# Performance work log

Measured on AMD Instinct MI355X. Metric: run time of the kernel, lower is better.

## Reference

```python
import jax, jax.numpy as jnp
import numpy as np
from jax import lax

B, CIN, HID, T, H, W = 4, 16, 16, 31, 128, 128


def setup_inputs() -> dict:
    key = jax.random.key(0)
    k1, k2 = jax.random.split(key)
    X = jax.random.normal(k1, (B, CIN, T, H, W), dtype=jnp.float32)
    # conv weight: Conv3d(in=16, out=4*hidden=64, k=3, pad=1), fan-in scaled
    fan_in = CIN * 27
    Wt = jax.random.normal(k2, (4 * HID, CIN, 3, 3, 3), dtype=jnp.float32) / np.sqrt(fan_in)
    b = jnp.zeros((4 * HID,), dtype=jnp.float32)
    return {"X": X, "W": Wt, "b": b}


def reference(X, W, b):
    # conv step: [B, 4*HID, T, H, W]
    gates = lax.conv_general_dilated(
        X, W, window_strides=(1, 1, 1), padding="SAME",
        dimension_numbers=("NCDHW", "OIDHW", "NCDHW"))
    gates = gates + b[None, :, None, None, None]
    Z, F, O, I = jnp.split(gates, 4, axis=1)
    Z = jnp.tanh(Z)
    F = jax.nn.sigmoid(F)
    O = jax.nn.sigmoid(O)
    I = jax.nn.sigmoid(I)

    # linear recurrence over time (axis=2), forward direction:
    # c_t = f_t * c_{t-1} + i_t * z_t  (c_{-1} = 0), h_t = o_t * c_t
    Zt = jnp.moveaxis(Z, 2, 0)  # [T, B, HID, H, W]
    Ft = jnp.moveaxis(F, 2, 0)
    Ot = jnp.moveaxis(O, 2, 0)
    It = jnp.moveaxis(I, 2, 0)

    def step(c, zfio):
        z, f, o, i = zfio
        c_ = f * c + i * z
        return c_, o * c_

    c0 = jnp.zeros_like(Zt[0])
    _, hs = lax.scan(step, c0, (Zt, Ft, Ot, It))
    return jnp.moveaxis(hs, 0, 2)  # [B, HID, T, H, W]
```

## Files before the change

### kernel.cpp

```cpp
#include <hip/hip_runtime.h>
#include <math.h>

#define Bn   4
#define CINn 16
#define HIDn 16
#define Tn   31
#define Hn   128
#define Wn   128

#define NS   14

typedef _Float16 half8 __attribute__((ext_vector_type(8)));
typedef float    f32x4 __attribute__((ext_vector_type(4)));

constexpr int KDt[28] = {0,0,0,0,0,0,0,0,0, 1,1,1,1,1,1,1,1,1, 2,2,2,2,2,2,2,2,2, 2};
constexpr int KHt[28] = {0,0,0,1,1,1,2,2,2, 0,0,0,1,1,1,2,2,2, 0,0,0,1,1,1,2,2,2, 2};
constexpr int KWt[28] = {0,1,2,0,1,2,0,1,2, 0,1,2,0,1,2,0,1,2, 0,1,2,0,1,2,0,1,2, 2};

__device__ __forceinline__ float sigmoidf_(float x) { return 1.f / (1.f + __expf(-x)); }
__device__ __forceinline__ float tanhf_(float x)    { return 2.f / (1.f + __expf(-2.f * x)) - 1.f; }

__global__ void repack_wa_kernel(const float* __restrict__ W, _Float16* __restrict__ WA) {
    int idx = blockIdx.x * blockDim.x + threadIdx.x;
    if (idx >= NS * 4 * 64 * 8) return;
    int j    = idx & 7;
    int lane = (idx >> 3) & 63;
    int m    = (idx >> 9) & 3;
    int s    = idx >> 11;
    int g    = lane >> 4;
    int tap  = 2 * s + (g >> 1);
    int cin  = (g & 1) * 8 + j;
    int oc   = m * 16 + (lane & 15);
    float v  = (tap < 27) ? W[(size_t)(oc * CINn + cin) * 27 + tap] : 0.f;
    WA[idx] = (_Float16)v;
}

#define POSB    32
#define ROWF    (130*POSB)
#define SLOTF   (3*ROWF)
#define LDSF    (4*SLOTF)
#define XH_OFF  65536
#define SLICE_B (Hn*Wn*CINn*2)
#define WS_NEED ((size_t)XH_OFF + (size_t)Bn*Tn*SLICE_B)

__global__ __launch_bounds__(256)
void transpose_x_kernel(const float* __restrict__ X, _Float16* __restrict__ Xh) {
    int i   = blockIdx.x * 256 + threadIdx.x;
    int pos = i & 16383;
    int bu  = i >> 14;
    int b   = bu / 31;
    int u   = bu - b * 31;
    const float* src = X + ((size_t)(b * CINn) * Tn + u) * 16384 + pos;
    half8 h0, h1;
    #pragma unroll
    for (int c = 0; c < 8; c++) h0[c] = (_Float16)src[(size_t)c * (Tn * 16384)];
    #pragma unroll
    for (int c = 0; c < 8; c++) h1[c] = (_Float16)src[(size_t)(c + 8) * (Tn * 16384)];
    half8* dst = (half8*)(Xh + (size_t)i * 16);
    dst[0] = h0; dst[1] = h1;
}

__global__ __launch_bounds__(256, 2)
void qrnn_xh_kernel(const _Float16* __restrict__ Xh, const _Float16* __restrict__ WA,
                    const float* __restrict__ bias, float* __restrict__ out) {
    __shared__ __align__(16) char smem[LDSF];

    const int tid  = threadIdx.x;
    const int lane = tid & 63;
    const int wv   = tid >> 6;

    const int swz = (blockIdx.x & 7) * 64 + (blockIdx.x >> 3);
    const int b = swz >> 7;
    const int h = swz & 127;

    const size_t strideT = (size_t)Hn * Wn;
    const size_t strideC = (size_t)Tn * strideT;

    const int lane15  = lane & 15;
    const int g       = lane >> 4;
    const int ghi     = g >> 1;
    const int e       = g & 1;
    const int laneoff = lane15 * POSB + e * 16;
    const int wbase   = wv * 32;

    float bz[4], bfv[4], bov[4], biv[4];
    #pragma unroll
    for (int r = 0; r < 4; r++) {
        int hid = g * 4 + r;
        bz[r]  = bias[hid];
        bfv[r] = bias[HIDn + hid];
        bov[r] = bias[2 * HIDn + hid];
        biv[r] = bias[3 * HIDn + hid];
    }

    const char* XhB = (const char*)Xh + (size_t)b * Tn * SLICE_B;
    bool own[2], inb[2]; int soff[2], loff[2];
    #pragma unroll
    for (int k = 0; k < 2; k++) {
        int p  = tid + (k << 8);
        own[k] = (p < 3 * 130);
        int r    = (p >= 260) ? 2 : (p >= 130) ? 1 : 0;
        int wpos = p - r * 130;
        int hr = h - 1 + r;
        int wa = wpos - 1;
        inb[k]  = own[k] && (hr >= 0) && (hr < Hn) && (wa >= 0) && (wa < Wn);
        soff[k] = (hr * Wn + wa) * 32;
        loff[k] = r * ROWF + wpos * POSB;
    }

    half8 pfA[2], pfB[2];

    auto issue = [&](int u) {
        const bool uok = (u >= 0) && (u < Tn);
        #pragma unroll
        for (int k = 0; k < 2; k++) {
            half8 a = {}, c = {};
            if (uok && inb[k]) {
                const char* s = XhB + (size_t)u * SLICE_B + soff[k];
                a = *reinterpret_cast<const half8*>(s);
                c = *reinterpret_cast<const half8*>(s + 16);
            }
            pfA[k] = a; pfB[k] = c;
        }
    };
    auto commit = [&](int u) {
        char* sl = smem + (u & 3) * SLOTF;
        #pragma unroll
        for (int k = 0; k < 2; k++) if (own[k]) {
            *reinterpret_cast<half8*>(sl + loff[k])      = pfA[k];
            *reinterpret_cast<half8*>(sl + loff[k] + 16) = pfB[k];
        }
    };

    {
        half8 z = {};
        #pragma unroll
        for (int k = 0; k < 2; k++) if (own[k]) {
            *reinterpret_cast<half8*>(smem + 3 * SLOTF + loff[k])      = z;
            *reinterpret_cast<half8*>(smem + 3 * SLOTF + loff[k] + 16) = z;
        }
    }
    issue(0);
    commit(0);
    issue(1);

    float cst[2][4];
    #pragma unroll
    for (int n = 0; n < 2; n++)
        #pragma unroll
        for (int r = 0; r < 4; r++) cst[n][r] = 0.f;

    float* outb = out + (size_t)b * HIDn * strideC + (size_t)h * Wn + wbase + lane15;

    for (int t = 0; t < Tn; t++) {
        commit(t + 1);
        __syncthreads();
        issue(t + 2);

        const int sb[3] = { ((t + 3) & 3) * SLOTF, (t & 3) * SLOTF, ((t + 1) & 3) * SLOTF };

        f32x4 acc[2][4];
        #pragma unroll
        for (int n = 0; n < 2; n++)
            #pragma unroll
            for (int m = 0; m < 4; m++) acc[n][m] = (f32x4)(0.f);

        #pragma unroll
        for (int s = 0; s < NS; s++) {
            const half8 a0 = *reinterpret_cast<const half8*>(WA + ((size_t)(s * 4 + 0) * 64 + lane) * 8);
            const half8 a1 = *reinterpret_cast<const half8*>(WA + ((size_t)(s * 4 + 1) * 64 + lane) * 8);
            const half8 a2 = *reinterpret_cast<const half8*>(WA + ((size_t)(s * 4 + 2) * 64 + lane) * 8);
            const half8 a3 = *reinterpret_cast<const half8*>(WA + ((size_t)(s * 4 + 3) * 64 + lane) * 8);

            const int tA = 2 * s, tB = 2 * s + 1;
            const int offA = sb[KDt[tA]] + KHt[tA] * ROWF + KWt[tA] * POSB;
            const int offB = sb[KDt[tB]] + KHt[tB] * ROWF + KWt[tB] * POSB;
            const int off  = (ghi ? offB : offA) + laneoff;

            #pragma unroll
            for (int n = 0; n < 2; n++) {
                const half8 bf = *reinterpret_cast<const half8*>(
                    smem + off + (wbase + n * 16) * POSB);
                acc[n][0] = __builtin_amdgcn_mfma_f32_16x16x32_f16(a0, bf, acc[n][0], 0, 0, 0);
                acc[n][1] = __builtin_amdgcn_mfma_f32_16x16x32_f16(a1, bf, acc[n][1], 0, 0, 0);
                acc[n][2] = __builtin_amdgcn_mfma_f32_16x16x32_f16(a2, bf, acc[n][2], 0, 0, 0);
                acc[n][3] = __builtin_amdgcn_mfma_f32_16x16x32_f16(a3, bf, acc[n][3], 0, 0, 0);
            }
        }

        #pragma unroll
        for (int n = 0; n < 2; n++) {
            #pragma unroll
            for (int r = 0; r < 4; r++) {
                float z = tanhf_   (acc[n][0][r] + bz[r]);
                float f = sigmoidf_(acc[n][1][r] + bfv[r]);
                float o = sigmoidf_(acc[n][2][r] + bov[r]);
                float i = sigmoidf_(acc[n][3][r] + biv[r]);
                float c = f * cst[n][r] + i * z;
                cst[n][r] = c;
                outb[(size_t)(g * 4 + r) * strideC + (size_t)t * strideT + n * 16] = o * c;
            }
        }
    }
}

#define WSTR  48
#define ROWB  (130*WSTR)
#define SLOT3 (3*ROWB)
#define LDS3  (3*SLOT3)

__global__ __launch_bounds__(256, 2)
void qrnn_fb_kernel(const float* __restrict__ X, const _Float16* __restrict__ WA,
                    const float* __restrict__ bias, float* __restrict__ out) {
    __shared__ __align__(16) char smem[LDS3];
    const int tid  = threadIdx.x;
    const int lane = tid & 63;
    const int wv   = tid >> 6;
    const int swz = (blockIdx.x & 7) * 64 + (blockIdx.x >> 3);
    const int b = swz >> 7;
    const int h = swz & 127;
    const size_t strideT = (size_t)Hn * Wn;
    const size_t strideC = (size_t)Tn * strideT;
    const float* Xb = X + (size_t)b * CINn * strideC;
    const int lane15  = lane & 15;
    const int g       = lane >> 4;
    const int ghi     = g >> 1;
    const int laneoff = lane15 * WSTR + (g & 1) * 16;
    const int wbase   = wv * 32;
    float bz[4], bfv[4], bov[4], biv[4];
    #pragma unroll
    for (int r = 0; r < 4; r++) {
        int hid = g * 4 + r;
        bz[r] = bias[hid]; bfv[r] = bias[HIDn + hid];
        bov[r] = bias[2 * HIDn + hid]; biv[r] = bias[3 * HIDn + hid];
    }
    auto stage = [&](int u, int s) {
        const bool uok = (u >= 0) && (u < Tn);
        for (int p = tid; p < 3 * 130; p += 256) {
            int row  = (p >= 260) ? 2 : (p >= 130) ? 1 : 0;
            int wpos = p - row * 130;
            int hr = h - 1 + row;
            int wa = wpos - 1;
            bool valid = uok && (hr >= 0) && (hr < Hn) && (wa >= 0) && (wa < Wn);
            const float* src = Xb + (ptrdiff_t)u * (ptrdiff_t)strideT + (ptrdiff_t)hr * Wn + wa;
            half8 h0, h1;
            #pragma unroll
            for (int c8 = 0; c8 < 8; c8++) h0[c8] = valid ? (_Float16)src[(size_t)c8 * strideC] : (_Float16)0.f;
            #pragma unroll
            for (int c8 = 0; c8 < 8; c8++) h1[c8] = valid ? (_Float16)src[(size_t)(8 + c8) * strideC] : (_Float16)0.f;
            char* dst = smem + s * SLOT3 + row * ROWB + wpos * WSTR;
            *reinterpret_cast<half8*>(dst)      = h0;
            *reinterpret_cast<half8*>(dst + 16) = h1;
        }
    };
    float cst[2][4];
    #pragma unroll
    for (int n = 0; n < 2; n++)
        #pragma unroll
        for (int r = 0; r < 4; r++) cst[n][r] = 0.f;
    stage(-1, 2);
    stage(0, 0);
    float* outb = out + (size_t)b * HIDn * strideC + (size_t)h * Wn + wbase + lane15;
    for (int t = 0; t < Tn; t++) {
        stage(t + 1, (t + 1) % 3);
        __syncthreads();
        const int sb[3] = { ((t + 2) % 3) * SLOT3, (t % 3) * SLOT3, ((t + 1) % 3) * SLOT3 };
        f32x4 acc[2][4];
        #pragma unroll
        for (int n = 0; n < 2; n++)
            #pragma unroll
            for (int m = 0; m < 4; m++) acc[n][m] = (f32x4)(0.f);
        #pragma unroll
        for (int s = 0; s < NS; s++) {
            const half8 a0 = *reinterpret_cast<const half8*>(WA + ((size_t)(s * 4 + 0) * 64 + lane) * 8);
            const half8 a1 = *reinterpret_cast<const half8*>(WA + ((size_t)(s * 4 + 1) * 64 + lane) * 8);
            const half8 a2 = *reinterpret_cast<const half8*>(WA + ((size_t)(s * 4 + 2) * 64 + lane) * 8);
            const half8 a3 = *reinterpret_cast<const half8*>(WA + ((size_t)(s * 4 + 3) * 64 + lane) * 8);
            const int tA = 2 * s, tB = 2 * s + 1;
            const int offA = sb[KDt[tA]] + KHt[tA] * ROWB + KWt[tA] * WSTR;
            const int offB = sb[KDt[tB]] + KHt[tB] * ROWB + KWt[tB] * WSTR;
            const int off  = (ghi ? offB : offA) + laneoff;
            #pragma unroll
            for (int n = 0; n < 2; n++) {
                const half8 bf = *reinterpret_cast<const half8*>(smem + off + (wbase + n * 16) * WSTR);
                acc[n][0] = __builtin_amdgcn_mfma_f32_16x16x32_f16(a0, bf, acc[n][0], 0, 0, 0);
                acc[n][1] = __builtin_amdgcn_mfma_f32_16x16x32_f16(a1, bf, acc[n][1], 0, 0, 0);
                acc[n][2] = __builtin_amdgcn_mfma_f32_16x16x32_f16(a2, bf, acc[n][2], 0, 0, 0);
                acc[n][3] = __builtin_amdgcn_mfma_f32_16x16x32_f16(a3, bf, acc[n][3], 0, 0, 0);
            }
        }
        #pragma unroll
        for (int n = 0; n < 2; n++) {
            #pragma unroll
            for (int r = 0; r < 4; r++) {
                float z = tanhf_   (acc[n][0][r] + bz[r]);
                float f = sigmoidf_(acc[n][1][r] + bfv[r]);
                float o = sigmoidf_(acc[n][2][r] + bov[r]);
                float i = sigmoidf_(acc[n][3][r] + biv[r]);
                float c = f * cst[n][r] + i * z;
                cst[n][r] = c;
                outb[(size_t)(g * 4 + r) * strideC + (size_t)t * strideT + n * 16] = o * c;
            }
        }
        __syncthreads();
    }
}

extern "C" void kernel_launch(void* const* d_in, const int* in_sizes, int n_in,
                              void* d_out, int out_size, void* d_ws, size_t ws_size,
                              hipStream_t stream) {
    const float* X    = (const float*)d_in[0];
    const float* W    = (const float*)d_in[1];
    const float* bias = (const float*)d_in[2];
    float* out = (float*)d_out;

    _Float16* WA = (_Float16*)d_ws;
    repack_wa_kernel<<<(NS * 4 * 64 * 8 + 255) / 256, 256, 0, stream>>>(W, WA);

    if (ws_size >= WS_NEED) {
        _Float16* Xh = (_Float16*)((char*)d_ws + XH_OFF);
        transpose_x_kernel<<<(Bn * Tn * Hn * Wn) / 256, 256, 0, stream>>>(X, Xh);
        qrnn_xh_kernel<<<Bn * Hn, 256, 0, stream>>>(Xh, WA, bias, out);
    } else {
        qrnn_fb_kernel<<<Bn * Hn, 256, 0, stream>>>(X, WA, bias, out);
    }
}
```

Baseline: 484.6 us.

## Split each image row across two blocks and pad LDS positions to reduce conflicts

The main conv-recurrence kernel now assigns half a row (64 columns) to each block, doubling the grid to 1024 blocks. Each wave handles 16 columns instead of 32, so accumulators and LDS tiles shrink, and launch bounds are raised to allow 4 blocks per CU. The LDS position stride grows from 32 to 48 bytes, which is meant to spread accesses across banks. In exchange, the halo columns are loaded twice across neighbouring blocks, and each block spends proportionally more time on staging and barrier overhead relative to its compute.

```diff
diff --git a/kernel.cpp b/kernel.cpp
--- a/kernel.cpp
+++ b/kernel.cpp
@@ -35,10 +35,12 @@
     WA[idx] = (_Float16)v;
 }
 
-#define POSB    32
-#define ROWF    (130*POSB)
+#define POSB    48
+#define NWPOS   66
+#define ROWF    (NWPOS*POSB)
 #define SLOTF   (3*ROWF)
 #define LDSF    (4*SLOTF)
+#define NPOS    (3*NWPOS)
 #define XH_OFF  65536
 #define SLICE_B (Hn*Wn*CINn*2)
 #define WS_NEED ((size_t)XH_OFF + (size_t)Bn*Tn*SLICE_B)
@@ -60,7 +62,7 @@
     dst[0] = h0; dst[1] = h1;
 }
 
-__global__ __launch_bounds__(256, 2)
+__global__ __launch_bounds__(256, 4)
 void qrnn_xh_kernel(const _Float16* __restrict__ Xh, const _Float16* __restrict__ WA,
                     const float* __restrict__ bias, float* __restrict__ out) {
     __shared__ __align__(16) char smem[LDSF];
@@ -69,19 +71,21 @@
     const int lane = tid & 63;
     const int wv   = tid >> 6;
 
-    const int swz = (blockIdx.x & 7) * 64 + (blockIdx.x >> 3);
-    const int b = swz >> 7;
-    const int h = swz & 127;
+    const int swz = (blockIdx.x & 7) * 128 + (blockIdx.x >> 3);
+    const int b    = swz >> 8;
+    const int h    = (swz >> 1) & 127;
+    const int wh   = swz & 1;
+    const int woff = wh * 64;
 
     const size_t strideT = (size_t)Hn * Wn;
     const size_t strideC = (size_t)Tn * strideT;
 
-    const int lane15  = lane & 15;
-    const int g       = lane >> 4;
-    const int ghi     = g >> 1;
-    const int e       = g & 1;
-    const int laneoff = lane15 * POSB + e * 16;
-    const int wbase   = wv * 32;
+    const int lane15 = lane & 15;
+    const int g      = lane >> 4;
+    const int ghi    = g >> 1;
+    const int e      = g & 1;
+    const int wloc   = wv * 16 + lane15;
+    const int pbase  = wloc * POSB + e * 16;
 
     float bz[4], bfv[4], bov[4], biv[4];
     #pragma unroll
@@ -94,63 +98,46 @@
     }
 
     const char* XhB = (const char*)Xh + (size_t)b * Tn * SLICE_B;
-    bool own[2], inb[2]; int soff[2], loff[2];
-    #pragma unroll
-    for (int k = 0; k < 2; k++) {
-        int p  = tid + (k << 8);
-        own[k] = (p < 3 * 130);
-        int r    = (p >= 260) ? 2 : (p >= 130) ? 1 : 0;
-        int wpos = p - r * 130;
-        int hr = h - 1 + r;
-        int wa = wpos - 1;
-        inb[k]  = own[k] && (hr >= 0) && (hr < Hn) && (wa >= 0) && (wa < Wn);
-        soff[k] = (hr * Wn + wa) * 32;
-        loff[k] = r * ROWF + wpos * POSB;
-    }
-
-    half8 pfA[2], pfB[2];
+    const bool own  = (tid < NPOS);
+    const int  srow = tid / NWPOS;
+    const int  swp  = tid - srow * NWPOS;
+    const int  hr   = h - 1 + srow;
+    const int  wa   = woff - 1 + swp;
+    const bool inb  = own && (hr >= 0) && (hr < Hn) && (wa >= 0) && (wa < Wn);
+    const int  soff = (hr * Wn + wa) * 32;
+    const int  loff = srow * ROWF + swp * POSB;
+
+    half8 pfA, pfB;
 
     auto issue = [&](int u) {
-        const bool uok = (u >= 0) && (u < Tn);
-        #pragma unroll
-        for (int k = 0; k < 2; k++) {
-            half8 a = {}, c = {};
-            if (uok && inb[k]) {
-                const char* s = XhB + (size_t)u * SLICE_B + soff[k];
-                a = *reinterpret_cast<const half8*>(s);
-                c = *reinterpret_cast<const half8*>(s + 16);
-            }
-            pfA[k] = a; pfB[k] = c;
-        }
+        half8 a = {}, c = {};
+        if (inb && u >= 0 && u < Tn) {
+            const char* s = XhB + (size_t)u * SLICE_B + soff;
+            a = *reinterpret_cast<const half8*>(s);
+            c = *reinterpret_cast<const half8*>(s + 16);
+        }
+        pfA = a; pfB = c;
     };
     auto commit = [&](int u) {
-        char* sl = smem + (u & 3) * SLOTF;
-        #pragma unroll
-        for (int k = 0; k < 2; k++) if (own[k]) {
-            *reinterpret_cast<half8*>(sl + loff[k])      = pfA[k];
-            *reinterpret_cast<half8*>(sl + loff[k] + 16) = pfB[k];
+        if (own) {
+            char* dst = smem + (u & 3) * SLOTF + loff;
+            *reinterpret_cast<half8*>(dst)      = pfA;
+            *reinterpret_cast<half8*>(dst + 16) = pfB;
         }
     };
 
-    {
+    if (own) {
         half8 z = {};
-        #pragma unroll
-        for (int k = 0; k < 2; k++) if (own[k]) {
-            *reinterpret_cast<half8*>(smem + 3 * SLOTF + loff[k])      = z;
-            *reinterpret_cast<half8*>(smem + 3 * SLOTF + loff[k] + 16) = z;
-        }
+        char* dst = smem + 3 * SLOTF + loff;
+        *reinterpret_cast<half8*>(dst)      = z;
+        *reinterpret_cast<half8*>(dst + 16) = z;
     }
     issue(0);
     commit(0);
     issue(1);
 
-    float cst[2][4];
-    #pragma unroll
-    for (int n = 0; n < 2; n++)
-        #pragma unroll
-        for (int r = 0; r < 4; r++) cst[n][r] = 0.f;
-
-    float* outb = out + (size_t)b * HIDn * strideC + (size_t)h * Wn + wbase + lane15;
+    float cst[4] = {0.f, 0.f, 0.f, 0.f};
+    float* outb = out + (size_t)b * HIDn * strideC + (size_t)h * Wn + woff + wloc;
 
     for (int t = 0; t < Tn; t++) {
         commit(t + 1);
@@ -159,11 +146,9 @@
 
         const int sb[3] = { ((t + 3) & 3) * SLOTF, (t & 3) * SLOTF, ((t + 1) & 3) * SLOTF };
 
-        f32x4 acc[2][4];
-        #pragma unroll
-        for (int n = 0; n < 2; n++)
-            #pragma unroll
-            for (int m = 0; m < 4; m++) acc[n][m] = (f32x4)(0.f);
+        f32x4 acc[4];
+        #pragma unroll
+        for (int m = 0; m < 4; m++) acc[m] = (f32x4)(0.f);
 
         #pragma unroll
         for (int s = 0; s < NS; s++) {
@@ -175,31 +160,24 @@
             const int tA = 2 * s, tB = 2 * s + 1;
             const int offA = sb[KDt[tA]] + KHt[tA] * ROWF + KWt[tA] * POSB;
             const int offB = sb[KDt[tB]] + KHt[tB] * ROWF + KWt[tB] * POSB;
-            const int off  = (ghi ? offB : offA) + laneoff;
-
-            #pragma unroll
-            for (int n = 0; n < 2; n++) {
-                const half8 bf = *reinterpret_cast<const half8*>(
-                    smem + off + (wbase + n * 16) * POSB);
-                acc[n][0] = __builtin_amdgcn_mfma_f32_16x16x32_f16(a0, bf, acc[n][0], 0, 0, 0);
-                acc[n][1] = __builtin_amdgcn_mfma_f32_16x16x32_f16(a1, bf, acc[n][1], 0, 0, 0);
-                acc[n][2] = __builtin_amdgcn_mfma_f32_16x16x32_f16(a2, bf, acc[n][2], 0, 0, 0);
-                acc[n][3] = __builtin_amdgcn_mfma_f32_16x16x32_f16(a3, bf, acc[n][3], 0, 0, 0);
-            }
-        }
-
-        #pragma unroll
-        for (int n = 0; n < 2; n++) {
-            #pragma unroll
-            for (int r = 0; r < 4; r++) {
-                float z = tanhf_   (acc[n][0][r] + bz[r]);
-                float f = sigmoidf_(acc[n][1][r] + bfv[r]);
-                float o = sigmoidf_(acc[n][2][r] + bov[r]);
-                float i = sigmoidf_(acc[n][3][r] + biv[r]);
-                float c = f * cst[n][r] + i * z;
-                cst[n][r] = c;
-                outb[(size_t)(g * 4 + r) * strideC + (size_t)t * strideT + n * 16] = o * c;
-            }
+            const int off  = (ghi ? offB : offA) + pbase;
+
+            const half8 bf = *reinterpret_cast<const half8*>(smem + off);
+            acc[0] = __builtin_amdgcn_mfma_f32_16x16x32_f16(a0, bf, acc[0], 0, 0, 0);
+            acc[1] = __builtin_amdgcn_mfma_f32_16x16x32_f16(a1, bf, acc[1], 0, 0, 0);
+            acc[2] = __builtin_amdgcn_mfma_f32_16x16x32_f16(a2, bf, acc[2], 0, 0, 0);
+            acc[3] = __builtin_amdgcn_mfma_f32_16x16x32_f16(a3, bf, acc[3], 0, 0, 0);
+        }
+
+        #pragma unroll
+        for (int r = 0; r < 4; r++) {
+            float z = tanhf_   (acc[0][r] + bz[r]);
+            float f = sigmoidf_(acc[1][r] + bfv[r]);
+            float o = sigmoidf_(acc[2][r] + bov[r]);
+            float i = sigmoidf_(acc[3][r] + biv[r]);
+            float c = f * cst[r] + i * z;
+            cst[r] = c;
+            outb[(size_t)(g * 4 + r) * strideC + (size_t)t * strideT] = o * c;
         }
     }
 }
@@ -320,7 +298,7 @@
     if (ws_size >= WS_NEED) {
         _Float16* Xh = (_Float16*)((char*)d_ws + XH_OFF);
         transpose_x_kernel<<<(Bn * Tn * Hn * Wn) / 256, 256, 0, stream>>>(X, Xh);
-        qrnn_xh_kernel<<<Bn * Hn, 256, 0, stream>>>(Xh, WA, bias, out);
+        qrnn_xh_kernel<<<Bn * Hn * 2, 256, 0, stream>>>(Xh, WA, bias, out);
     } else {
         qrnn_fb_kernel<<<Bn * Hn, 256, 0, stream>>>(X, WA, bias, out);
     }
```

Measured after the change: 987.6 us. 2.04x slower.
